# Kernel tuning notes

Measured on AMD Instinct MI355X. Metric: run time of the kernel, lower is better.

The kernel has to match this reference:

```python
import jax, jax.numpy as jnp
import numpy as np

B, N, K, V = 16, 256, 2048, 768

def setup_inputs() -> dict:
    key = jax.random.key(0)
    k1, k2 = jax.random.split(key)
    inputs = jax.random.normal(k1, (B, N, V), dtype=jnp.float32)
    prototypes = jax.random.normal(k2, (K, V), dtype=jnp.float32)
    return {"inputs": inputs, "prototypes": prototypes}

def reference(inputs, prototypes):
    # distances[b,n,k] = sum_v (inputs[b,n,v] - prototypes[k,v])**2
    x_sq = jnp.sum(inputs * inputs, axis=-1, keepdims=True)          # [B,N,1]
    p_sq = jnp.sum(prototypes * prototypes, axis=-1)                  # [K]
    xp = jnp.einsum("bnv,kv->bnk", inputs, prototypes)               # [B,N,K]
    distances = x_sq + p_sq[None, None, :] - 2.0 * xp
    return (distances, prototypes)
```

## Files before the change

kernel.cpp:

```cpp
#include <hip/hip_runtime.h>
#include <hip/hip_bf16.h>
#include <stdint.h>

#define Kdim 2048
#define Vdim 768
#define Mdim 4096

#define NT 12

typedef __attribute__((ext_vector_type(8))) short short8;
typedef __attribute__((ext_vector_type(16))) float f32x16;

#define CFENCE asm volatile("" ::: "memory")

struct alignas(8) B4 { __hip_bfloat16 a, b, c, d; };

__global__ __launch_bounds__(256, 2) void fused_dist(const float* __restrict__ x,
                                                     const float* __restrict__ p,
                                                     float* __restrict__ out) {
    __shared__ __hip_bfloat16 Asb[2][128 * 64];
    __shared__ __hip_bfloat16 Bsb[2][128 * 64];

    const int t = threadIdx.x;
    const int lane = t & 63;
    const int wave = t >> 6;
    const int wr = wave >> 1;
    const int wc = wave & 1;
    const int ln31 = lane & 31;
    const int lh = lane >> 5;

    const int wg = (blockIdx.x & 7) * 64 + (blockIdx.x >> 3);
    const int bm = wg >> 4, bn = wg & 15;
    const int m0 = bm * 128, n0 = bn * 128;

    const int rg = t >> 4;
    const int c16 = t & 15;
    const float* Axp = x + (size_t)(m0 + rg) * Vdim + c16 * 4;
    const float* Bxp = p + (size_t)(n0 + rg) * Vdim + c16 * 4;

    int woff[8];
#pragma unroll
    for (int j = 0; j < 8; ++j) {
        const int r = rg + 16 * j;
        woff[j] = r * 128 + (((c16 >> 1) ^ (r & 7)) << 4) + (c16 & 1) * 8;
    }

    int offA[2][4], offB[2][4];
#pragma unroll
    for (int mt = 0; mt < 2; ++mt)
#pragma unroll
        for (int ks = 0; ks < 4; ++ks) {
            const int S = ks * 2 + lh;
            const int rA = wr * 64 + mt * 32 + ln31;
            const int rB = wc * 64 + mt * 32 + ln31;
            offA[mt][ks] = rA * 128 + ((S ^ (rA & 7)) << 4);
            offB[mt][ks] = rB * 128 + ((S ^ (rB & 7)) << 4);
        }

    float4 pa[8], pb[8];
    float aacc[8] = {0, 0, 0, 0, 0, 0, 0, 0};
    float bacc[8] = {0, 0, 0, 0, 0, 0, 0, 0};
    f32x16 acc[2][2] = {};

    auto LOAD = [&](int kt) {
#pragma unroll
        for (int j = 0; j < 8; ++j) {
            pa[j] = *reinterpret_cast<const float4*>(Axp + (size_t)(16 * j) * Vdim + kt * 64);
            pb[j] = *reinterpret_cast<const float4*>(Bxp + (size_t)(16 * j) * Vdim + kt * 64);
        }
    };
    auto QW = [&](int buf) {
        char* As = reinterpret_cast<char*>(&Asb[buf][0]);
        char* Bsl = reinterpret_cast<char*>(&Bsb[buf][0]);
#pragma unroll
        for (int j = 0; j < 8; ++j) {
            float4 v = pa[j];
            aacc[j] = fmaf(v.x, v.x, fmaf(v.y, v.y, fmaf(v.z, v.z, fmaf(v.w, v.w, aacc[j]))));
            B4 w;
            w.a = __float2bfloat16(v.x); w.b = __float2bfloat16(v.y);
            w.c = __float2bfloat16(v.z); w.d = __float2bfloat16(v.w);
            *reinterpret_cast<B4*>(As + woff[j]) = w;
            float4 u = pb[j];
            bacc[j] = fmaf(u.x, u.x, fmaf(u.y, u.y, fmaf(u.z, u.z, fmaf(u.w, u.w, bacc[j]))));
            B4 z;
            z.a = __float2bfloat16(u.x); z.b = __float2bfloat16(u.y);
            z.c = __float2bfloat16(u.z); z.d = __float2bfloat16(u.w);
            *reinterpret_cast<B4*>(Bsl + woff[j]) = z;
        }
    };

    LOAD(0);
    QW(0);
    LOAD(1);
    asm volatile("s_waitcnt lgkmcnt(0)" ::: "memory");
    __builtin_amdgcn_s_barrier();
    CFENCE;

    for (int kt = 0; kt < NT; ++kt) {
        const int cb = kt & 1;
        if (kt + 1 < NT) QW(cb ^ 1);
        if (kt + 2 < NT) LOAD(kt + 2);
        CFENCE;

        const char* Ap = reinterpret_cast<const char*>(&Asb[cb][0]);
        const char* Bp = reinterpret_cast<const char*>(&Bsb[cb][0]);
        __builtin_amdgcn_s_setprio(1);
#pragma unroll
        for (int ks = 0; ks < 4; ++ks) {
            short8 af0 = *reinterpret_cast<const short8*>(Ap + offA[0][ks]);
            short8 af1 = *reinterpret_cast<const short8*>(Ap + offA[1][ks]);
            short8 bf0 = *reinterpret_cast<const short8*>(Bp + offB[0][ks]);
            short8 bf1 = *reinterpret_cast<const short8*>(Bp + offB[1][ks]);
            acc[0][0] = __builtin_amdgcn_mfma_f32_32x32x16_bf16(af0, bf0, acc[0][0], 0, 0, 0);
            acc[0][1] = __builtin_amdgcn_mfma_f32_32x32x16_bf16(af0, bf1, acc[0][1], 0, 0, 0);
            acc[1][0] = __builtin_amdgcn_mfma_f32_32x32x16_bf16(af1, bf0, acc[1][0], 0, 0, 0);
            acc[1][1] = __builtin_amdgcn_mfma_f32_32x32x16_bf16(af1, bf1, acc[1][1], 0, 0, 0);
        }
        __builtin_amdgcn_s_setprio(0);
        CFENCE;
        asm volatile("s_waitcnt lgkmcnt(0)" ::: "memory");
        __builtin_amdgcn_s_barrier();
        CFENCE;
    }

    {
        const int prow = n0 + bm * 4 + wave;
        const float* srcp = p + (size_t)prow * Vdim;
        float* dstp = out + (size_t)Mdim * Kdim + (size_t)prow * Vdim;
#pragma unroll
        for (int i = 0; i < 3; ++i)
            *reinterpret_cast<float4*>(dstp + i * 256 + lane * 4) =
                *reinterpret_cast<const float4*>(srcp + i * 256 + lane * 4);
    }

    float* scr = reinterpret_cast<float*>(&Asb[0][0]);
#pragma unroll
    for (int j = 0; j < 8; ++j) {
        scr[(rg + 16 * j) * 16 + c16] = aacc[j];
        scr[2048 + (rg + 16 * j) * 16 + c16] = bacc[j];
    }
    asm volatile("s_waitcnt lgkmcnt(0)" ::: "memory");
    __builtin_amdgcn_s_barrier();
    float* rowsum = reinterpret_cast<float*>(&Bsb[0][0]);
    {
        const float* base = scr + (t < 128 ? t * 16 : 2048 + (t - 128) * 16);
        float s = 0.f;
#pragma unroll
        for (int c = 0; c < 16; ++c) s += base[c];
        rowsum[t] = s;
    }
    asm volatile("s_waitcnt lgkmcnt(0)" ::: "memory");
    __builtin_amdgcn_s_barrier();

    float ps_[2];
    int col_[2];
#pragma unroll
    for (int nt = 0; nt < 2; ++nt) {
        const int cl = wc * 64 + nt * 32 + ln31;
        col_[nt] = n0 + cl;
        ps_[nt] = rowsum[128 + cl];
    }
#pragma unroll
    for (int mt = 0; mt < 2; ++mt)
#pragma unroll
        for (int reg = 0; reg < 16; ++reg) {
            const int rowl = wr * 64 + mt * 32 + (reg & 3) + 8 * (reg >> 2) + 4 * lh;
            const float xs = rowsum[rowl];
#pragma unroll
            for (int nt = 0; nt < 2; ++nt)
                out[(size_t)(m0 + rowl) * Kdim + col_[nt]] =
                    xs + ps_[nt] - 2.0f * acc[mt][nt][reg];
        }
}

extern "C" void kernel_launch(void* const* d_in, const int* in_sizes, int n_in,
                              void* d_out, int out_size, void* d_ws, size_t ws_size,
                              hipStream_t stream) {
    const float* x = (const float*)d_in[0];
    const float* p = (const float*)d_in[1];
    float* out = (float*)d_out;

    fused_dist<<<512, 256, 0, stream>>>(x, p, out);
}
```

Measured before the change: 33.94 us.

## Enlarge block tile to 256x128 with 512 threads and manual double-buffer unroll

Result: no change. 33.86 us (-0.3%).

```diff
diff --git a/kernel.cpp b/kernel.cpp
--- a/kernel.cpp
+++ b/kernel.cpp
@@ -15,11 +15,10 @@
 
 struct alignas(8) B4 { __hip_bfloat16 a, b, c, d; };
 
-__global__ __launch_bounds__(256, 2) void fused_dist(const float* __restrict__ x,
+__global__ __launch_bounds__(512, 1) void fused_dist(const float* __restrict__ x,
                                                      const float* __restrict__ p,
                                                      float* __restrict__ out) {
-    __shared__ __hip_bfloat16 Asb[2][128 * 64];
-    __shared__ __hip_bfloat16 Bsb[2][128 * 64];
+    __shared__ char lds[98304];
 
     const int t = threadIdx.x;
     const int lane = t & 63;
@@ -29,20 +28,26 @@
     const int ln31 = lane & 31;
     const int lh = lane >> 5;
 
-    const int wg = (blockIdx.x & 7) * 64 + (blockIdx.x >> 3);
-    const int bm = wg >> 4, bn = wg & 15;
-    const int m0 = bm * 128, n0 = bn * 128;
+    const int xcd = blockIdx.x & 7, seq = blockIdx.x >> 3;
+    const int bn = seq >> 1;
+    const int bm = 2 * xcd + (seq & 1);
+    const int m0 = bm * 256, n0 = bn * 128;
 
     const int rg = t >> 4;
     const int c16 = t & 15;
     const float* Axp = x + (size_t)(m0 + rg) * Vdim + c16 * 4;
     const float* Bxp = p + (size_t)(n0 + rg) * Vdim + c16 * 4;
 
-    int woff[8];
+    int woffA[8], woffB[4];
 #pragma unroll
     for (int j = 0; j < 8; ++j) {
-        const int r = rg + 16 * j;
-        woff[j] = r * 128 + (((c16 >> 1) ^ (r & 7)) << 4) + (c16 & 1) * 8;
+        const int r = rg + 32 * j;
+        woffA[j] = r * 128 + (((c16 >> 1) ^ (r & 7)) << 4) + (c16 & 1) * 8;
+    }
+#pragma unroll
+    for (int j = 0; j < 4; ++j) {
+        const int r = rg + 32 * j;
+        woffB[j] = r * 128 + (((c16 >> 1) ^ (r & 7)) << 4) + (c16 & 1) * 8;
     }
 
     int offA[2][4], offB[2][4];
@@ -57,100 +62,102 @@
             offB[mt][ks] = rB * 128 + ((S ^ (rB & 7)) << 4);
         }
 
-    float4 pa[8], pb[8];
-    float aacc[8] = {0, 0, 0, 0, 0, 0, 0, 0};
-    float bacc[8] = {0, 0, 0, 0, 0, 0, 0, 0};
+    float4 R0[12], R1[12];
+    float aacc[8] = {0,0,0,0,0,0,0,0};
+    float bacc[4] = {0,0,0,0};
     f32x16 acc[2][2] = {};
 
-    auto LOAD = [&](int kt) {
-#pragma unroll
-        for (int j = 0; j < 8; ++j) {
-            pa[j] = *reinterpret_cast<const float4*>(Axp + (size_t)(16 * j) * Vdim + kt * 64);
-            pb[j] = *reinterpret_cast<const float4*>(Bxp + (size_t)(16 * j) * Vdim + kt * 64);
-        }
-    };
-    auto QW = [&](int buf) {
-        char* As = reinterpret_cast<char*>(&Asb[buf][0]);
-        char* Bsl = reinterpret_cast<char*>(&Bsb[buf][0]);
-#pragma unroll
-        for (int j = 0; j < 8; ++j) {
-            float4 v = pa[j];
-            aacc[j] = fmaf(v.x, v.x, fmaf(v.y, v.y, fmaf(v.z, v.z, fmaf(v.w, v.w, aacc[j]))));
-            B4 w;
-            w.a = __float2bfloat16(v.x); w.b = __float2bfloat16(v.y);
-            w.c = __float2bfloat16(v.z); w.d = __float2bfloat16(v.w);
-            *reinterpret_cast<B4*>(As + woff[j]) = w;
-            float4 u = pb[j];
-            bacc[j] = fmaf(u.x, u.x, fmaf(u.y, u.y, fmaf(u.z, u.z, fmaf(u.w, u.w, bacc[j]))));
-            B4 z;
-            z.a = __float2bfloat16(u.x); z.b = __float2bfloat16(u.y);
-            z.c = __float2bfloat16(u.z); z.d = __float2bfloat16(u.w);
-            *reinterpret_cast<B4*>(Bsl + woff[j]) = z;
-        }
-    };
+#define LOADX(kt, S) do {                                                         \
+    _Pragma("unroll") for (int j = 0; j < 8; ++j)                                 \
+        S[j] = *reinterpret_cast<const float4*>(Axp + (size_t)(32 * j) * Vdim + (kt) * 64); \
+    _Pragma("unroll") for (int j = 0; j < 4; ++j)                                 \
+        S[8 + j] = *reinterpret_cast<const float4*>(Bxp + (size_t)(32 * j) * Vdim + (kt) * 64); \
+} while (0)
 
-    LOAD(0);
-    QW(0);
-    LOAD(1);
-    asm volatile("s_waitcnt lgkmcnt(0)" ::: "memory");
-    __builtin_amdgcn_s_barrier();
-    CFENCE;
+#define QWX(S, buf) do {                                                          \
+    char* Ad = lds + (buf) * 32768;                                               \
+    char* Bd = lds + 65536 + (buf) * 16384;                                       \
+    _Pragma("unroll") for (int j = 0; j < 8; ++j) {                               \
+        float4 v = S[j];                                                          \
+        aacc[j] = fmaf(v.x, v.x, fmaf(v.y, v.y, fmaf(v.z, v.z, fmaf(v.w, v.w, aacc[j])))); \
+        B4 w; w.a = __float2bfloat16(v.x); w.b = __float2bfloat16(v.y);           \
+        w.c = __float2bfloat16(v.z); w.d = __float2bfloat16(v.w);                 \
+        *reinterpret_cast<B4*>(Ad + woffA[j]) = w; }                              \
+    _Pragma("unroll") for (int j = 0; j < 4; ++j) {                               \
+        float4 v = S[8 + j];                                                      \
+        bacc[j] = fmaf(v.x, v.x, fmaf(v.y, v.y, fmaf(v.z, v.z, fmaf(v.w, v.w, bacc[j])))); \
+        B4 w; w.a = __float2bfloat16(v.x); w.b = __float2bfloat16(v.y);           \
+        w.c = __float2bfloat16(v.z); w.d = __float2bfloat16(v.w);                 \
+        *reinterpret_cast<B4*>(Bd + woffB[j]) = w; }                              \
+} while (0)
 
-    for (int kt = 0; kt < NT; ++kt) {
-        const int cb = kt & 1;
-        if (kt + 1 < NT) QW(cb ^ 1);
-        if (kt + 2 < NT) LOAD(kt + 2);
+#define MSTEP(buf) do {                                                           \
+    const char* Ap = lds + (buf) * 32768;                                         \
+    const char* Bp = lds + 65536 + (buf) * 16384;                                 \
+    __builtin_amdgcn_s_setprio(1);                                                \
+    _Pragma("unroll") for (int ks = 0; ks < 4; ++ks) {                            \
+        short8 a0 = *reinterpret_cast<const short8*>(Ap + offA[0][ks]);           \
+        short8 a1 = *reinterpret_cast<const short8*>(Ap + offA[1][ks]);           \
+        short8 b0 = *reinterpret_cast<const short8*>(Bp + offB[0][ks]);           \
+        short8 b1 = *reinterpret_cast<const short8*>(Bp + offB[1][ks]);           \
+        acc[0][0] = __builtin_amdgcn_mfma_f32_32x32x16_bf16(a0, b0, acc[0][0], 0, 0, 0); \
+        acc[0][1] = __builtin_amdgcn_mfma_f32_32x32x16_bf16(a0, b1, acc[0][1], 0, 0, 0); \
+        acc[1][0] = __builtin_amdgcn_mfma_f32_32x32x16_bf16(a1, b0, acc[1][0], 0, 0, 0); \
+        acc[1][1] = __builtin_amdgcn_mfma_f32_32x32x16_bf16(a1, b1, acc[1][1], 0, 0, 0); } \
+    __builtin_amdgcn_s_setprio(0);                                                \
+} while (0)
+
+#define BARRIER do {                                                              \
+    asm volatile("s_waitcnt lgkmcnt(0)" ::: "memory");                            \
+    __builtin_amdgcn_s_barrier();                                                 \
+    CFENCE;                                                                       \
+} while (0)
+
+    LOADX(0, R0);
+    QWX(R0, 0);
+    LOADX(1, R1);
+    BARRIER;
+
+    for (int kt = 0; kt < NT; kt += 2) {
+        if (kt + 2 < NT) LOADX(kt + 2, R0);
+        if (kt + 1 < NT) QWX(R1, 1);
         CFENCE;
-
-        const char* Ap = reinterpret_cast<const char*>(&Asb[cb][0]);
-        const char* Bp = reinterpret_cast<const char*>(&Bsb[cb][0]);
-        __builtin_amdgcn_s_setprio(1);
-#pragma unroll
-        for (int ks = 0; ks < 4; ++ks) {
-            short8 af0 = *reinterpret_cast<const short8*>(Ap + offA[0][ks]);
-            short8 af1 = *reinterpret_cast<const short8*>(Ap + offA[1][ks]);
-            short8 bf0 = *reinterpret_cast<const short8*>(Bp + offB[0][ks]);
-            short8 bf1 = *reinterpret_cast<const short8*>(Bp + offB[1][ks]);
-            acc[0][0] = __builtin_amdgcn_mfma_f32_32x32x16_bf16(af0, bf0, acc[0][0], 0, 0, 0);
-            acc[0][1] = __builtin_amdgcn_mfma_f32_32x32x16_bf16(af0, bf1, acc[0][1], 0, 0, 0);
-            acc[1][0] = __builtin_amdgcn_mfma_f32_32x32x16_bf16(af1, bf0, acc[1][0], 0, 0, 0);
-            acc[1][1] = __builtin_amdgcn_mfma_f32_32x32x16_bf16(af1, bf1, acc[1][1], 0, 0, 0);
-        }
-        __builtin_amdgcn_s_setprio(0);
+        MSTEP(0);
         CFENCE;
-        asm volatile("s_waitcnt lgkmcnt(0)" ::: "memory");
-        __builtin_amdgcn_s_barrier();
+        BARRIER;
+        if (kt + 3 < NT) LOADX(kt + 3, R1);
+        if (kt + 2 < NT) QWX(R0, 0);
         CFENCE;
+        MSTEP(1);
+        CFENCE;
+        BARRIER;
     }
 
     {
-        const int prow = n0 + bm * 4 + wave;
-        const float* srcp = p + (size_t)prow * Vdim;
-        float* dstp = out + (size_t)Mdim * Kdim + (size_t)prow * Vdim;
+        const int pr = blockIdx.x * 8 + (t >> 6);
+        const float* srcp = p + (size_t)pr * Vdim;
+        float* dstp = out + (size_t)Mdim * Kdim + (size_t)pr * Vdim;
 #pragma unroll
         for (int i = 0; i < 3; ++i)
-            *reinterpret_cast<float4*>(dstp + i * 256 + lane * 4) =
-                *reinterpret_cast<const float4*>(srcp + i * 256 + lane * 4);
+            *reinterpret_cast<float4*>(dstp + (t & 63) * 4 + i * 256) =
+                *reinterpret_cast<const float4*>(srcp + (t & 63) * 4 + i * 256);
     }
 
-    float* scr = reinterpret_cast<float*>(&Asb[0][0]);
+    float* scr = reinterpret_cast<float*>(lds);
 #pragma unroll
-    for (int j = 0; j < 8; ++j) {
-        scr[(rg + 16 * j) * 16 + c16] = aacc[j];
-        scr[2048 + (rg + 16 * j) * 16 + c16] = bacc[j];
-    }
-    asm volatile("s_waitcnt lgkmcnt(0)" ::: "memory");
-    __builtin_amdgcn_s_barrier();
-    float* rowsum = reinterpret_cast<float*>(&Bsb[0][0]);
-    {
-        const float* base = scr + (t < 128 ? t * 16 : 2048 + (t - 128) * 16);
+    for (int j = 0; j < 8; ++j) scr[(rg + 32 * j) * 17 + c16] = aacc[j];
+#pragma unroll
+    for (int j = 0; j < 4; ++j) scr[4352 + (rg + 32 * j) * 17 + c16] = bacc[j];
+    BARRIER;
+    float* rowsum = reinterpret_cast<float*>(lds + 65536);
+    if (t < 384) {
+        const float* base = scr + (t < 256 ? t * 17 : 4352 + (t - 256) * 17);
         float s = 0.f;
 #pragma unroll
         for (int c = 0; c < 16; ++c) s += base[c];
         rowsum[t] = s;
     }
-    asm volatile("s_waitcnt lgkmcnt(0)" ::: "memory");
-    __builtin_amdgcn_s_barrier();
+    BARRIER;
 
     float ps_[2];
     int col_[2];
@@ -158,7 +165,7 @@
     for (int nt = 0; nt < 2; ++nt) {
         const int cl = wc * 64 + nt * 32 + ln31;
         col_[nt] = n0 + cl;
-        ps_[nt] = rowsum[128 + cl];
+        ps_[nt] = rowsum[256 + cl];
     }
 #pragma unroll
     for (int mt = 0; mt < 2; ++mt)
@@ -171,6 +178,10 @@
                 out[(size_t)(m0 + rowl) * Kdim + col_[nt]] =
                     xs + ps_[nt] - 2.0f * acc[mt][nt][reg];
         }
+#undef LOADX
+#undef QWX
+#undef MSTEP
+#undef BARRIER
 }
 
 extern "C" void kernel_launch(void* const* d_in, const int* in_sizes, int n_in,
@@ -180,5 +191,5 @@
     const float* p = (const float*)d_in[1];
     float* out = (float*)d_out;
 
-    fused_dist<<<512, 256, 0, stream>>>(x, p, out);
+    fused_dist<<<256, 512, 0, stream>>>(x, p, out);
 }
```
